# Kernel tuning notes

Measured on AMD Instinct MI355X. Metric: run time of the kernel, lower is better.

The kernel has to match this reference:

```python
import jax, jax.numpy as jnp
import numpy as np

B, L, LP, N, D, H, NL = 8, 24, 48, 325, 128, 8, 3
DFF = 4 * D          # d_ff = 4*d_model
ORDER, SUP = 2, 2    # diffusion order, support_len (1 static + 1 adaptive)
KC = ORDER * SUP + 1 # 5 concatenated diffusion channels
E = D // H


def setup_inputs() -> dict:
    key = jax.random.key(0)
    ks = iter(jax.random.split(key, 48))
    g = lambda shape: jax.random.normal(next(ks), shape, dtype=jnp.float32) * 0.02
    return {
        "x": jax.random.normal(next(ks), (B, L, N, D), dtype=jnp.float32),
        "memory": jax.random.normal(next(ks), (B, LP, N, D), dtype=jnp.float32),
        "data": jax.random.normal(next(ks), (B, L, N, D), dtype=jnp.float32),
        "support": jax.random.uniform(next(ks), (N, N), dtype=jnp.float32) / N,
        # [layer, 0=self/1=cross, ...] attention projections
        "Wq": g((NL, 2, D, D)), "bq": jnp.zeros((NL, 2, D), jnp.float32),
        "Wk": g((NL, 2, D, D)), "bk": jnp.zeros((NL, 2, D), jnp.float32),
        "Wv": g((NL, 2, D, D)), "bv": jnp.zeros((NL, 2, D), jnp.float32),
        "Wo": g((NL, 2, D, D)), "bo": jnp.zeros((NL, 2, D), jnp.float32),
        "W1": g((NL, D, DFF)), "b1": jnp.zeros((NL, DFF), jnp.float32),
        "W2": g((NL, DFF, D)), "b2": jnp.zeros((NL, D), jnp.float32),
        "W3": g((NL, D, N)),   "b3": jnp.zeros((NL, N), jnp.float32),
        "lng": jnp.ones((NL, 3, D), jnp.float32), "lnb": jnp.zeros((NL, 3, D), jnp.float32),
        # one GCN (1x1-conv mlp) per output timestep per layer
        "gcnW": g((NL, L, KC * D, D)), "gcnb": jnp.zeros((NL, L, D), jnp.float32),
        "skW": g((NL, D, D)), "skb": jnp.zeros((NL, D), jnp.float32),
        "outg": jnp.ones((D,), jnp.float32), "outb": jnp.zeros((D,), jnp.float32),
    }


def _ln(x, g, b, eps=1e-5):
    mu = x.mean(-1, keepdims=True)
    xc = x - mu
    v = (xc * xc).mean(-1, keepdims=True)
    return xc * jax.lax.rsqrt(v + eps) * g + b


def _lin_attn(qx, kx, Wq, bq, Wk, bk, Wv, bv, Wo, bo):
    # linear attention with elu+1 feature map over flattened (time*node) tokens
    Bq, S, _ = qx.shape
    T = kx.shape[1]
    q = (qx @ Wq + bq).reshape(Bq, S, H, E)
    k = (kx @ Wk + bk).reshape(Bq, T, H, E)
    v = (kx @ Wv + bv).reshape(Bq, T, H, E)
    qp = jax.nn.elu(q) + 1.0
    kp = jax.nn.elu(k) + 1.0
    kv = jnp.einsum('bthe,bthd->bhed', kp, v)
    z = 1.0 / (jnp.einsum('bshe,bhe->bsh', qp, kp.sum(1)) + 1e-6)
    out = jnp.einsum('bshe,bhed,bsh->bshd', qp, kv, z).reshape(Bq, S, D)
    return out @ Wo + bo


def _forward(x, memory, data, support, Wq, bq, Wk, bk, Wv, bv, Wo, bo,
             W1, b1, W2, b2, W3, b3, lng, lnb, gcnW, gcnb, skW, skb, outg, outb):
    skip = 0.0
    dtm = data.transpose(0, 1, 3, 2)          # [B,L,C=D,N] channels-first node features
    s1 = jnp.einsum('blcn,nm->blcm', dtm, support)
    s2 = jnp.einsum('blcn,nm->blcm', s1, support)
    for i in range(NL):
        # self-attention (tokens = L*N)
        xf = x.reshape(B, L * N, D)
        sa = _lin_attn(xf, xf, Wq[i, 0], bq[i, 0], Wk[i, 0], bk[i, 0],
                       Wv[i, 0], bv[i, 0], Wo[i, 0], bo[i, 0])
        x = _ln(x + sa.reshape(B, L, N, D), lng[i, 0], lnb[i, 0])
        # cross-attention to memory (tokens = LP*N)
        xf = x.reshape(B, L * N, D)
        mf = memory.reshape(B, LP * N, D)
        ca = _lin_attn(xf, mf, Wq[i, 1], bq[i, 1], Wk[i, 1], bk[i, 1],
                       Wv[i, 1], bv[i, 1], Wo[i, 1], bo[i, 1])
        x = _ln(x + ca.reshape(B, L, N, D), lng[i, 1], lnb[i, 1])
        # FFN + adaptive adjacency head
        y = jax.nn.gelu(jnp.einsum('blnd,df->blnf', x, W1[i]) + b1[i], approximate=False)
        y = jnp.einsum('blnf,fd->blnd', y, W2[i]) + b2[i]
        As = jnp.einsum('blnd,dm->blnm', y, W3[i]) + b3[i]   # [B,L,N,N] per-step adjacency
        # multi-support diffusion GCN, vectorized over all L timesteps
        a1 = jnp.einsum('blcn,blnm->blcm', dtm, As)
        a2 = jnp.einsum('blcn,blnm->blcm', a1, As)
        h = jnp.concatenate([dtm, s1, s2, a1, a2], axis=2)   # [B,L,KC*D,N]
        dts = jnp.einsum('blcn,lco->blno', h, gcnW[i]) + gcnb[i][None, :, None, :]
        x = _ln(x + y, lng[i, 2], lnb[i, 2])
        # 1x1 skip conv + accumulate
        skip = skip + jnp.einsum('blnd,do->blno', dts, skW[i]) + skb[i]
    return _ln(jax.nn.relu(skip), outg, outb)


def reference(x, memory, data, support, Wq, bq, Wk, bk, Wv, bv, Wo, bo,
              W1, b1, W2, b2, W3, b3, lng, lnb, gcnW, gcnb, skW, skb, outg, outb):
    return _forward(x, memory, data, support, Wq, bq, Wk, bk, Wv, bv, Wo, bo,
                    W1, b1, W2, b2, W3, b3, lng, lnb, gcnW, gcnb, skW, skb, outg, outb)
```

## Files before the change

kernel.cpp:

```cpp
#include <hip/hip_runtime.h>
#include <hip/hip_bf16.h>
#include <math.h>

#define B_   8
#define L_   24
#define LP_  48
#define N_   325
#define D_   128
#define H_   8
#define NL_  3
#define DFF_ 512

typedef __attribute__((ext_vector_type(8))) short s16x8;
typedef __attribute__((ext_vector_type(4))) float f32x4;
typedef __hip_bfloat16 bf16;

static const int  ROWS    = B_ * L_ * N_;
static const int  T_SELF  = L_ * N_;
static const int  T_CROSS = LP_ * N_;
static const long long U_ = (long long)T_SELF * D_;
static const long long SZ = (long long)B_ * U_;

enum { EPI_NONE = 0, EPI_ELU1 = 1, EPI_GELU = 2 };

struct MOut { void* d[3]; int ldc_[3]; int flg[3]; };

__device__ __forceinline__ float apply_epi(float v, int epi) {
    if (epi == EPI_ELU1) return (v > 0.f) ? (v + 1.f) : expf(v);
    if (epi == EPI_GELU) return 0.5f * v * (1.f + erff(v * 0.70710678118654752f));
    return v;
}

template<int ABF>
__global__ __launch_bounds__(256) void gk64(
    const void* __restrict__ Av, const bf16* __restrict__ Bt,
    const float* __restrict__ bias, void* __restrict__ Cv,
    int M, int Nc, int K,
    long long sA, long long sB, long long sC,
    int lda, int ldb, int ldc,
    int bmod, long long sBias, int accum, int epi, int obf, int rowbias, int npad)
{
    const int batch = blockIdx.z;
    const int m0 = blockIdx.x * 64, n0 = blockIdx.y * 64;
    const int tid = threadIdx.x, lane = tid & 63;
    const int w = tid >> 6, wm = w >> 1, wn = w & 1;
    const int r16 = lane & 15, kb = lane >> 4;

    __shared__ __align__(16) bf16 shm[64 * 144];

    const float* Af = ABF ? nullptr : ((const float*)Av + (long long)batch * sA);
    const bf16*  Ab = ABF ? ((const bf16*)Av + (long long)batch * sA) : nullptr;
    const bf16*  Bp = Bt + (long long)(batch % bmod) * sB;

    f32x4 acc[2][2];
#pragma unroll
    for (int i = 0; i < 2; ++i)
#pragma unroll
        for (int j = 0; j < 2; ++j) acc[i][j] = f32x4{0.f, 0.f, 0.f, 0.f};

    for (int k0 = 0; k0 < K; k0 += 64) {
#pragma unroll
        for (int s = 0; s < 2; ++s) {
            int slot = tid + s * 256;
            int row = slot >> 3, kg = slot & 7;
            int m = m0 + row, k = k0 + kg * 8;
            union { s16x8 v; bf16 h[8]; } val;
            if (m < M) {
                if (ABF) {
                    val.v = *(const s16x8*)(Ab + (long long)m * lda + k);
                } else {
                    f32x4 v0 = *(const f32x4*)(Af + (long long)m * lda + k);
                    f32x4 v1 = *(const f32x4*)(Af + (long long)m * lda + k + 4);
#pragma unroll
                    for (int e = 0; e < 4; ++e) {
                        val.h[e]     = __float2bfloat16(v0[e]);
                        val.h[e + 4] = __float2bfloat16(v1[e]);
                    }
                }
            } else {
#pragma unroll
                for (int e = 0; e < 8; ++e) val.h[e] = __float2bfloat16(0.f);
            }
            *(s16x8*)&shm[row * 72 + kg * 8] = val.v;
        }
#pragma unroll
        for (int s = 0; s < 2; ++s) {
            int slot = tid + s * 256;
            int row = slot >> 3, kg = slot & 7;
            int n = n0 + row, k = k0 + kg * 8;
            union { s16x8 v; bf16 h[8]; } val;
            if (n < Nc) {
                val.v = *(const s16x8*)(Bp + (long long)n * ldb + k);
            } else {
#pragma unroll
                for (int e = 0; e < 8; ++e) val.h[e] = __float2bfloat16(0.f);
            }
            *(s16x8*)&shm[4608 + row * 72 + kg * 8] = val.v;
        }
        __syncthreads();
#pragma unroll
        for (int kh = 0; kh < 2; ++kh) {
            s16x8 av[2], bv[2];
#pragma unroll
            for (int mi = 0; mi < 2; ++mi)
                av[mi] = *(const s16x8*)&shm[(wm * 32 + mi * 16 + r16) * 72 + kh * 32 + kb * 8];
#pragma unroll
            for (int ni = 0; ni < 2; ++ni)
                bv[ni] = *(const s16x8*)&shm[4608 + (wn * 32 + ni * 16 + r16) * 72 + kh * 32 + kb * 8];
#pragma unroll
            for (int mi = 0; mi < 2; ++mi)
#pragma unroll
                for (int ni = 0; ni < 2; ++ni)
                    acc[mi][ni] = __builtin_amdgcn_mfma_f32_16x16x32_bf16(
                        av[mi], bv[ni], acc[mi][ni], 0, 0, 0);
        }
        __syncthreads();
    }

    const float* bp = bias ? (bias + (long long)(batch % bmod) * sBias) : nullptr;
    if (obf) {
        bf16* Cb = (bf16*)Cv + (long long)batch * sC;
#pragma unroll
        for (int mi = 0; mi < 2; ++mi)
#pragma unroll
            for (int ni = 0; ni < 2; ++ni)
#pragma unroll
                for (int rr = 0; rr < 4; ++rr) {
                    int row = wm * 32 + mi * 16 + kb * 4 + rr;
                    int col = wn * 32 + ni * 16 + r16;
                    int m = m0 + row, n = n0 + col;
                    float v = 0.f;
                    if (m < M && n < Nc) {
                        v = acc[mi][ni][rr];
                        if (bp) v += rowbias ? bp[m] : bp[n];
                        v = apply_epi(v, epi);
                    }
                    shm[row * 72 + col] = __float2bfloat16(v);
                }
        __syncthreads();
#pragma unroll
        for (int it = 0; it < 2; ++it) {
            int row = (tid >> 3) + it * 32;
            int col = (tid & 7) * 8;
            int m = m0 + row, nglob = n0 + col;
            if (m < M && nglob < npad)
                *(s16x8*)(Cb + (long long)m * ldc + nglob) = *(const s16x8*)&shm[row * 72 + col];
        }
        return;
    }

    float* Cf = (float*)Cv + (long long)batch * sC;
#pragma unroll
    for (int mi = 0; mi < 2; ++mi) {
#pragma unroll
        for (int ni = 0; ni < 2; ++ni) {
#pragma unroll
            for (int rr = 0; rr < 4; ++rr) {
                int m = m0 + wm * 32 + mi * 16 + kb * 4 + rr;
                int n = n0 + wn * 32 + ni * 16 + r16;
                if (m >= M || n >= Nc) continue;
                float v = acc[mi][ni][rr];
                if (bp) v += rowbias ? bp[m] : bp[n];
                v = apply_epi(v, epi);
                long long ci = (long long)m * ldc + n;
                if (accum) Cf[ci] += v; else Cf[ci] = v;
            }
        }
    }
}

template<int ABF>
__global__ __launch_bounds__(256) void gk64m(
    const void* __restrict__ Av, const bf16* __restrict__ Bt,
    const float* __restrict__ bias, MOut mo, int M, int K, int lda, int ldb)
{
    const int bn = blockIdx.y;
    const int m0 = blockIdx.x * 64, n0 = bn * 64;
    const int tid = threadIdx.x, lane = tid & 63;
    const int w = tid >> 6, wm = w >> 1, wn = w & 1;
    const int r16 = lane & 15, kb = lane >> 4;

    __shared__ __align__(16) bf16 shm[64 * 144];

    const float* Af = ABF ? nullptr : (const float*)Av;
    const bf16*  Ab = ABF ? (const bf16*)Av : nullptr;

    f32x4 acc[2][2];
#pragma unroll
    for (int i = 0; i < 2; ++i)
#pragma unroll
        for (int j = 0; j < 2; ++j) acc[i][j] = f32x4{0.f, 0.f, 0.f, 0.f};

    for (int k0 = 0; k0 < K; k0 += 64) {
#pragma unroll
        for (int s = 0; s < 2; ++s) {
            int slot = tid + s * 256;
            int row = slot >> 3, kg = slot & 7;
            int m = m0 + row, k = k0 + kg * 8;
            union { s16x8 v; bf16 h[8]; } val;
            if (m < M) {
                if (ABF) {
                    val.v = *(const s16x8*)(Ab + (long long)m * lda + k);
                } else {
                    f32x4 v0 = *(const f32x4*)(Af + (long long)m * lda + k);
                    f32x4 v1 = *(const f32x4*)(Af + (long long)m * lda + k + 4);
#pragma unroll
                    for (int e = 0; e < 4; ++e) {
                        val.h[e]     = __float2bfloat16(v0[e]);
                        val.h[e + 4] = __float2bfloat16(v1[e]);
                    }
                }
            } else {
#pragma unroll
                for (int e = 0; e < 8; ++e) val.h[e] = __float2bfloat16(0.f);
            }
            *(s16x8*)&shm[row * 72 + kg * 8] = val.v;
        }
#pragma unroll
        for (int s = 0; s < 2; ++s) {
            int slot = tid + s * 256;
            int row = slot >> 3, kg = slot & 7;
            int n = n0 + row, k = k0 + kg * 8;
            *(s16x8*)&shm[4608 + row * 72 + kg * 8] =
                *(const s16x8*)(Bt + (long long)n * ldb + k);
        }
        __syncthreads();
#pragma unroll
        for (int kh = 0; kh < 2; ++kh) {
            s16x8 av[2], bv[2];
#pragma unroll
            for (int mi = 0; mi < 2; ++mi)
                av[mi] = *(const s16x8*)&shm[(wm * 32 + mi * 16 + r16) * 72 + kh * 32 + kb * 8];
#pragma unroll
            for (int ni = 0; ni < 2; ++ni)
                bv[ni] = *(const s16x8*)&shm[4608 + (wn * 32 + ni * 16 + r16) * 72 + kh * 32 + kb * 8];
#pragma unroll
            for (int mi = 0; mi < 2; ++mi)
#pragma unroll
                for (int ni = 0; ni < 2; ++ni)
                    acc[mi][ni] = __builtin_amdgcn_mfma_f32_16x16x32_bf16(
                        av[mi], bv[ni], acc[mi][ni], 0, 0, 0);
        }
        __syncthreads();
    }

    const int oi = bn >> 1;
    const int epi_ = mo.flg[oi];
    bf16* Cb = (bf16*)mo.d[oi];
    const int ldcc = mo.ldc_[oi];
    const int cbase = (bn & 1) * 64;
#pragma unroll
    for (int mi = 0; mi < 2; ++mi)
#pragma unroll
        for (int ni = 0; ni < 2; ++ni)
#pragma unroll
            for (int rr = 0; rr < 4; ++rr) {
                int row = wm * 32 + mi * 16 + kb * 4 + rr;
                int col = wn * 32 + ni * 16 + r16;
                int m = m0 + row;
                float v = 0.f;
                if (m < M) {
                    v = acc[mi][ni][rr] + bias[n0 + col];
                    v = apply_epi(v, epi_);
                }
                shm[row * 72 + col] = __float2bfloat16(v);
            }
    __syncthreads();
#pragma unroll
    for (int it = 0; it < 2; ++it) {
        int row = (tid >> 3) + it * 32;
        int col = (tid & 7) * 8;
        int m = m0 + row;
        if (m < M)
            *(s16x8*)(Cb + (long long)m * ldcc + cbase + col) = *(const s16x8*)&shm[row * 72 + col];
    }
}

static inline void gemm64(hipStream_t st, int abf, const void* A, const bf16* Bt,
                          const float* bias, void* C,
                          int M, int Nc, int K,
                          long long sA, long long sB, long long sC,
                          int lda, int ldb, int ldc,
                          int z, int bmod, long long sBias, int accum, int epi, int obf,
                          int rowbias = 0, int npad = 0)
{
    if (npad < Nc) npad = Nc;
    dim3 g((M + 63) / 64, (npad + 63) / 64, z);
    if (abf) gk64<1><<<g,256,0,st>>>(A,Bt,bias,C,M,Nc,K,sA,sB,sC,lda,ldb,ldc,bmod,sBias,accum,epi,obf,rowbias,npad);
    else     gk64<0><<<g,256,0,st>>>(A,Bt,bias,C,M,Nc,K,sA,sB,sC,lda,ldb,ldc,bmod,sBias,accum,epi,obf,rowbias,npad);
}

static inline void gemm3_64(hipStream_t st, int abf, const void* A, const bf16* Bt,
                            const float* bias, const MOut& mo, int M, int Nc, int K,
                            int lda, int ldb)
{
    dim3 g((M + 63) / 64, Nc / 64, 1);
    if (abf) gk64m<1><<<g,256,0,st>>>(A,Bt,bias,mo,M,K,lda,ldb);
    else     gk64m<0><<<g,256,0,st>>>(A,Bt,bias,mo,M,K,lda,ldb);
}

template<int SBF>
__global__ __launch_bounds__(256) void tconv(
    const void* __restrict__ srcv, bf16* __restrict__ dst,
    int R, int C, int lds_, long long sS, int rbound, int drs, long long sD)
{
    const int bz = blockIdx.z;
    const float* sf = SBF ? nullptr : ((const float*)srcv + (long long)bz * sS);
    const bf16* sb = SBF ? ((const bf16*)srcv + (long long)bz * sS) : nullptr;
    bf16* dp = dst + (long long)bz * sD;
    __shared__ float t[32][33];
    const int r0 = blockIdx.x * 32, c0 = blockIdx.y * 32;
    for (int i = threadIdx.y; i < 32; i += 8) {
        int r = r0 + i, c = c0 + threadIdx.x;
        float v = 0.f;
        if (r < R && c < C)
            v = SBF ? __bfloat162float(sb[(long long)r * lds_ + c]) : sf[(long long)r * lds_ + c];
        t[i][threadIdx.x] = v;
    }
    __syncthreads();
    for (int i = threadIdx.y; i < 32; i += 8) {
        int c = c0 + i, r = r0 + threadIdx.x;
        if (c < C && r < rbound) dp[(long long)c * drs + r] = __float2bfloat16(t[threadIdx.x][i]);
    }
}

__global__ __launch_bounds__(256) void conv_k(
    const float* __restrict__ src, bf16* __restrict__ dst,
    long long total, int C, int slds, int dldd)
{
    for (long long idx = blockIdx.x * 256LL + threadIdx.x; idx < total;
         idx += (long long)gridDim.x * 256) {
        long long r = idx / C; int c = (int)(idx - r * C);
        dst[r * dldd + c] = __float2bfloat16(src[r * slds + c]);
    }
}

__global__ __launch_bounds__(256) void gsum_k(
    const bf16* __restrict__ gskt, bf16* __restrict__ gsum, long long per)
{
    for (long long j = blockIdx.x * 256LL + threadIdx.x; j < per;
         j += (long long)gridDim.x * 256) {
        float a = __bfloat162float(gskt[j]) + __bfloat162float(gskt[per + j])
                + __bfloat162float(gskt[2 * per + j]);
        gsum[j] = __float2bfloat16(a);
    }
}

__global__ __launch_bounds__(128) void bsk_k(
    const float* __restrict__ gcnb, const float* __restrict__ skW,
    const float* __restrict__ skb, float* __restrict__ out)
{
    const int l = blockIdx.x, o = threadIdx.x;
    float acc = 0.f;
    for (int i = 0; i < NL_; ++i) {
        acc += skb[i * 128 + o];
        const float* gb = gcnb + (i * 24 + l) * 128;
        const float* sw = skW + i * 16384;
        for (int c = 0; c < 128; ++c) acc += gb[c] * sw[c * 128 + o];
    }
    out[l * 128 + o] = acc;
}

__global__ __launch_bounds__(384) void cbias_k(
    const float* __restrict__ bq, const float* __restrict__ bk,
    const float* __restrict__ bv, float* __restrict__ bqkv)
{
    const int wi = blockIdx.x, j = threadIdx.x;
    float v = (j < 128) ? bq[wi * 128 + j] : (j < 256) ? bk[wi * 128 + j - 128] : bv[wi * 128 + j - 256];
    bqkv[wi * 384 + j] = v;
}

__global__ __launch_bounds__(256) void kv_part_bf16(
    const bf16* __restrict__ kp, const bf16* __restrict__ vp,
    float* __restrict__ part, int T, int TC)
{
    const int z = blockIdx.z, h = blockIdx.y, tc = blockIdx.x;
    kp += (long long)z * T * D_;
    vp += (long long)z * T * D_;
    const int t0 = tc * 512;
    const int tend = min(T, t0 + 512);
    const int tid = threadIdx.x;
    const int e = tid >> 4, d = tid & 15;
    __shared__ float sk[64][16];
    __shared__ float sv[64][16];
    float acc = 0.f, asum = 0.f;
    for (int tb = t0; tb < tend; tb += 64) {
#pragma unroll
        for (int r = 0; r < 4; ++r) {
            int idx = tid + r * 256, tt = idx >> 4, c = idx & 15;
            int t = tb + tt;
            float kk = 0.f, vv = 0.f;
            if (t < tend) {
                long long gi = (long long)t * D_ + h * 16 + c;
                kk = __bfloat162float(kp[gi]);
                vv = __bfloat162float(vp[gi]);
            }
            sk[tt][c] = kk; sv[tt][c] = vv;
        }
        __syncthreads();
#pragma unroll 8
        for (int tt = 0; tt < 64; ++tt) {
            float ke = sk[tt][e];
            acc  = fmaf(ke, sv[tt][d], acc);
            asum += ke;
        }
        __syncthreads();
    }
    float* pp = part + (((long long)z * TC + tc) * H_ + h) * 272;
    pp[e * 16 + d] = acc;
    if (d == 0) pp[256 + e] = asum;
}

__global__ __launch_bounds__(256) void kv_reduce2(
    const float* __restrict__ part, float* __restrict__ kv,
    float* __restrict__ ksum, int b0, int TC)
{
    const int h = blockIdx.x, z = blockIdx.y, b = b0 + z;
    const float* pz = part + (long long)z * TC * H_ * 272;
    const int tid = threadIdx.x, e = tid >> 4, d = tid & 15;
    float acc = 0.f;
    for (int tc = 0; tc < TC; ++tc) acc += pz[((long long)tc * H_ + h) * 272 + e * 16 + d];
    kv[((long long)(b * H_ + h) * 16 + e) * 16 + d] = acc;
    if (d == 0) {
        float s = 0.f;
        for (int tc = 0; tc < TC; ++tc) s += pz[((long long)tc * H_ + h) * 272 + 256 + e];
        ksum[(b * H_ + h) * 16 + e] = s;
    }
}

__global__ __launch_bounds__(256) void attn_out_bf(
    const bf16* __restrict__ qp, const float* __restrict__ kv,
    const float* __restrict__ ksum, bf16* __restrict__ out)
{
    const int row = blockIdx.x * 2 + threadIdx.y;
    const int o = threadIdx.x;
    const int h = o >> 4, dp = o & 15;
    __shared__ float sq[2][D_];
    const int b = row / T_SELF;
    sq[threadIdx.y][o] = __bfloat162float(qp[(long long)row * D_ + o]);
    __syncthreads();
    const float* ks  = ksum + (b * H_ + h) * 16;
    const float* kvp = kv + (long long)(b * H_ + h) * 256 + dp;
    float den = 1e-6f, acc = 0.f;
#pragma unroll
    for (int e = 0; e < 16; ++e) {
        float q = sq[threadIdx.y][h * 16 + e];
        den = fmaf(q, ks[e], den);
        acc = fmaf(q, kvp[e * 16], acc);
    }
    out[(long long)row * D_ + o] = __float2bfloat16(acc / den);
}

template<int XBF, int OBF>
__global__ __launch_bounds__(256) void addln_k(
    const void* __restrict__ xin, const bf16* __restrict__ addend,
    const float* __restrict__ g, const float* __restrict__ beta,
    void* __restrict__ outp, int relu_mode)
{
    const int row = blockIdx.x * 4 + threadIdx.y;
    const int lane = threadIdx.x;
    const long long base = (long long)row * D_;
    float v0, v1;
    if (XBF) {
        v0 = __bfloat162float(((const bf16*)xin)[base + lane]);
        v1 = __bfloat162float(((const bf16*)xin)[base + lane + 64]);
    } else {
        v0 = ((const float*)xin)[base + lane];
        v1 = ((const float*)xin)[base + lane + 64];
    }
    if (addend) {
        v0 += __bfloat162float(addend[base + lane]);
        v1 += __bfloat162float(addend[base + lane + 64]);
    }
    if (relu_mode) { v0 = fmaxf(v0, 0.f); v1 = fmaxf(v1, 0.f); }
    float s = v0 + v1;
#pragma unroll
    for (int off = 32; off; off >>= 1) s += __shfl_xor(s, off);
    const float mean = s * (1.f / 128.f);
    const float c0 = v0 - mean, c1 = v1 - mean;
    float vs = c0 * c0 + c1 * c1;
#pragma unroll
    for (int off = 32; off; off >>= 1) vs += __shfl_xor(vs, off);
    const float rstd = rsqrtf(vs * (1.f / 128.f) + 1e-5f);
    const float r0 = c0 * rstd * g[lane] + beta[lane];
    const float r1 = c1 * rstd * g[lane + 64] + beta[lane + 64];
    if (OBF) {
        ((bf16*)outp)[base + lane]      = __float2bfloat16(r0);
        ((bf16*)outp)[base + lane + 64] = __float2bfloat16(r1);
    } else {
        ((float*)outp)[base + lane]      = r0;
        ((float*)outp)[base + lane + 64] = r1;
    }
}

extern "C" void kernel_launch(void* const* d_in, const int* in_sizes, int n_in,
                              void* d_out, int out_size, void* d_ws, size_t ws_size,
                              hipStream_t stream)
{
    (void)in_sizes; (void)n_in; (void)out_size; (void)ws_size;

    const float* x_in    = (const float*)d_in[0];
    const float* mem     = (const float*)d_in[1];
    const float* data    = (const float*)d_in[2];
    const float* support = (const float*)d_in[3];
    const float* Wq  = (const float*)d_in[4];
    const float* bq  = (const float*)d_in[5];
    const float* Wk  = (const float*)d_in[6];
    const float* bk  = (const float*)d_in[7];
    const float* Wv  = (const float*)d_in[8];
    const float* bv  = (const float*)d_in[9];
    const float* Wo  = (const float*)d_in[10];
    const float* bo  = (const float*)d_in[11];
    const float* W1  = (const float*)d_in[12];
    const float* b1  = (const float*)d_in[13];
    const float* W2  = (const float*)d_in[14];
    const float* b2  = (const float*)d_in[15];
    const float* W3  = (const float*)d_in[16];
    const float* b3  = (const float*)d_in[17];
    const float* lng = (const float*)d_in[18];
    const float* lnb = (const float*)d_in[19];
    const float* gcnW= (const float*)d_in[20];
    const float* gcnb= (const float*)d_in[21];
    const float* skW = (const float*)d_in[22];
    const float* skb = (const float*)d_in[23];
    const float* outg= (const float*)d_in[24];
    const float* outb= (const float*)d_in[25];

    float* ws = (float*)d_ws;
    bf16*  Xb16 = (bf16*)ws;
    float* POOL = ws + 4000000LL;
    bf16*  PB   = (bf16*)POOL;
    bf16*  WBF  = (bf16*)(ws + 18800000LL);
    float* BQKV = ws + 23275008LL;
    float* BSK  = ws + 23277504LL;
    float* KVB  = ws + 23280576LL;
    float* KSB  = ws + 23296960LL;

    bf16* WQKVT = WBF + 0;
    bf16* WOT   = WBF + 294912;
    bf16* W1T   = WBF + 393216;
    bf16* W2T   = WBF + 589824;
    bf16* W3T   = WBF + 786432;
    bf16* SKWT  = WBF + 911232;
    bf16* SUPT  = WBF + 960384;
    bf16* GSKT  = WBF + 1085184;
    bf16* GSUM  = WBF + 6983424;

    float* SKIP = (float*)d_out;
    const int BIG = 1 << 30;
    dim3 blk(32, 8);
    auto TG = [](int rb, int C, int z) { return dim3((rb + 31) / 32, (C + 31) / 32, z); };

    tconv<0><<<TG(128,128,6),blk,0,stream>>>(Wq, WQKVT,          128,128,128, 16384, 128,128, 49152);
    tconv<0><<<TG(128,128,6),blk,0,stream>>>(Wk, WQKVT + 16384,  128,128,128, 16384, 128,128, 49152);
    tconv<0><<<TG(128,128,6),blk,0,stream>>>(Wv, WQKVT + 32768,  128,128,128, 16384, 128,128, 49152);
    tconv<0><<<TG(128,128,6),blk,0,stream>>>(Wo, WOT,            128,128,128, 16384, 128,128, 16384);
    tconv<0><<<TG(128,512,3),blk,0,stream>>>(W1, W1T,            128,512,512, 65536, 128,128, 65536);
    tconv<0><<<TG(512,128,3),blk,0,stream>>>(W2, W2T,            512,128,128, 65536, 512,512, 65536);
    tconv<0><<<TG(128,325,3),blk,0,stream>>>(W3, W3T,            128,325,325, 41600, 128,128, 41600);
    tconv<0><<<TG(128,128,3),blk,0,stream>>>(skW, SKWT,          128,128,128, 16384, 128,128, 16384);
    tconv<0><<<TG(384,325,1),blk,0,stream>>>(support, SUPT,      325,325,325, 0,     384,384, 0);
    bf16* gcnWbf = PB;
    conv_k<<<4096,256,0,stream>>>(gcnW, gcnWbf, 5898240LL, 128, 128, 128);
    for (int i = 0; i < NL_; ++i)
        gemm64(stream, 1, SKWT + i*16384, gcnWbf + (long long)i*1966080, nullptr,
               GSKT + (long long)i*1966080,
               128, 640, 128, 0, 81920, 81920, 128, 128, 640, 24, BIG, 0, 0, EPI_NONE, 1);
    gsum_k<<<2048,256,0,stream>>>(GSKT, GSUM, 1966080LL);
    bsk_k<<<24,128,0,stream>>>(gcnb, skW, skb, BSK);
    cbias_k<<<6,384,0,stream>>>(bq, bk, bv, BQKV);
    hipMemsetAsync(SKIP, 0, (size_t)SZ * sizeof(float), stream);

    for (int c = 0; c < 2; ++c) {
        const int b0 = c * 4;
        const float* datab = data + (long long)b0 * U_;
        bf16* Hs    = PB + 0;
        bf16* DTB   = PB + 12000000LL;
        bf16* s1_cm = PB + 16800000LL;
        conv_k<<<2048,256,0,stream>>>(datab, Hs, 96LL*41600, 128, 128, 384);
        tconv<0><<<TG(384,128,96),blk,0,stream>>>(datab, DTB, 325,128,128, 41600, 384,384, 49152);
        gemm64(stream, 1, DTB, SUPT, nullptr, s1_cm, 128,325,384,
               49152, 0, 49152, 384,384,384, 96, 1, 0, 0, EPI_NONE, 1, 0, 384);
        tconv<1><<<TG(128,325,96),blk,0,stream>>>(s1_cm, Hs + 128, 128,325,384, 49152, 128,384, 124800);
        gemm64(stream, 1, SUPT, s1_cm, nullptr, Hs + 256, 325,128,384,
               0, 49152, 124800, 384,384,384, 96, BIG, 0, 0, EPI_NONE, 1);
        gemm64(stream, 1, Hs, GSUM, BSK, SKIP + (long long)b0*U_,
               325,128,384, 124800, 81920, 41600, 384, 640, 128, 96, 24, 128, 1, EPI_NONE, 0);
    }

    for (int i = 0; i < NL_; ++i) {
        {
            const int wi = i * 2;
            bf16* Q  = PB + 0;
            bf16* KB = PB + 8000000LL;
            bf16* VB = PB + 16000000LL;
            float* PART = POOL + 12000000LL;
            bf16* OB = PB + 8000000LL;
            MOut mo{};
            mo.d[0] = Q;  mo.ldc_[0] = 128; mo.flg[0] = EPI_ELU1;
            mo.d[1] = KB; mo.ldc_[1] = 128; mo.flg[1] = EPI_ELU1;
            mo.d[2] = VB; mo.ldc_[2] = 128; mo.flg[2] = EPI_NONE;
            gemm3_64(stream, (i == 0) ? 0 : 1, (i == 0) ? (const void*)x_in : (const void*)Xb16,
                     WQKVT + (long long)wi*49152, BQKV + wi*384, mo, ROWS, 384, 128, 128, 128);
            kv_part_bf16<<<dim3(16,H_,8),256,0,stream>>>(KB, VB, PART, T_SELF, 16);
            kv_reduce2<<<dim3(H_,8),256,0,stream>>>(PART, KVB, KSB, 0, 16);
            attn_out_bf<<<ROWS/2, dim3(128,2),0,stream>>>(Q, KVB, KSB, Q);
            gemm64(stream, 1, Q, WOT + (long long)wi*16384, bo + wi*128, OB,
                   ROWS, 128, 128, 0,0,0, 128,128,128, 1,1,0, 0, EPI_NONE, 1);
            if (i == 0) addln_k<0,1><<<ROWS/4, dim3(64,4),0,stream>>>(
                x_in, OB, lng + (i*3)*128, lnb + (i*3)*128, Xb16, 0);
            else        addln_k<1,1><<<ROWS/4, dim3(64,4),0,stream>>>(
                Xb16, OB, lng + (i*3)*128, lnb + (i*3)*128, Xb16, 0);
        }

        {
            const int wi = i * 2 + 1;
            for (int c = 0; c < 2; ++c) {
                const int b0 = c * 4;
                bf16* KB = PB + 0;
                bf16* VB = PB + 8000000LL;
                float* PART = POOL + 12000000LL;
                MOut mo{};
                mo.d[0] = KB; mo.ldc_[0] = 128; mo.flg[0] = EPI_ELU1;
                mo.d[1] = VB; mo.ldc_[1] = 128; mo.flg[1] = EPI_NONE;
                gemm3_64(stream, 0, mem + (long long)b0 * T_CROSS * D_,
                         WQKVT + (long long)wi*49152 + 16384, BQKV + wi*384 + 128, mo,
                         4*T_CROSS, 256, 128, 128, 128);
                kv_part_bf16<<<dim3(31,H_,4),256,0,stream>>>(KB, VB, PART, T_CROSS, 31);
                kv_reduce2<<<dim3(H_,4),256,0,stream>>>(PART, KVB, KSB, b0, 31);
            }
            bf16* Q  = PB + 0;
            bf16* OB = PB + 8000000LL;
            gemm64(stream, 1, Xb16, WQKVT + (long long)wi*49152, BQKV + wi*384, Q,
                   ROWS, 128, 128, 0,0,0, 128,128,128, 1,1,0, 0, EPI_ELU1, 1);
            attn_out_bf<<<ROWS/2, dim3(128,2),0,stream>>>(Q, KVB, KSB, Q);
            gemm64(stream, 1, Q, WOT + (long long)wi*16384, bo + wi*128, OB,
                   ROWS, 128, 128, 0,0,0, 128,128,128, 1,1,0, 0, EPI_NONE, 1);
            addln_k<1,1><<<ROWS/4, dim3(64,4),0,stream>>>(
                Xb16, OB, lng + (i*3+1)*128, lnb + (i*3+1)*128, Xb16, 0);
        }

        for (int c = 0; c < 2; ++c) {
            const int b0 = c * 4;
            bf16* Xb = Xb16 + (long long)b0 * U_;

            bf16* FFH   = PB + 0;
            bf16* Ybf   = PB + 16000000LL;
            bf16* AST   = PB + 0;
            bf16* DTB   = PB + 12000000LL;
            bf16* a1_cm = PB + 16800000LL;
            bf16* Hd    = PB + 21600000LL;

            gemm64(stream, 1, Xb, W1T + (long long)i*65536, b1 + i*512, FFH,
                   4*T_SELF, 512, 128, 0,0,0, 128,128,512, 1,1,0, 0, EPI_GELU, 1);
            gemm64(stream, 1, FFH, W2T + (long long)i*65536, b2 + i*128, Ybf,
                   4*T_SELF, 128, 512, 0,0,0, 512,512,128, 1,1,0, 0, EPI_NONE, 1);
            addln_k<1,1><<<4*T_SELF/4, dim3(64,4),0,stream>>>(
                Xb, Ybf, lng + (i*3+2)*128, lnb + (i*3+2)*128, Xb, 0);
            gemm64(stream, 1, W3T + (long long)i*41600, Ybf, b3 + i*325, AST,
                   325, 325, 128, 0, 41600, 124800, 128, 128, 384, 96, BIG, 0, 0, EPI_NONE, 1, 1, 384);
            tconv<0><<<TG(384,128,96),blk,0,stream>>>(data + (long long)b0*U_, DTB,
                  325,128,128, 41600, 384,384, 49152);
            gemm64(stream, 1, DTB, AST, nullptr, a1_cm, 128,325,384,
                   49152, 124800, 49152, 384,384,384, 96, BIG, 0, 0, EPI_NONE, 1, 0, 384);
            tconv<1><<<TG(128,325,96),blk,0,stream>>>(a1_cm, Hd, 128,325,384, 49152, 128,256, 83200);
            gemm64(stream, 1, AST, a1_cm, nullptr, Hd + 128, 325,128,384,
                   124800, 49152, 83200, 384,384,256, 96, BIG, 0, 0, EPI_NONE, 1);
            gemm64(stream, 1, Hd, GSKT + (long long)i*1966080 + 384, nullptr,
                   SKIP + (long long)b0*U_, 325,128,256,
                   83200, 81920, 41600, 256, 640, 128, 96, 24, 0, 1, EPI_NONE, 0);
        }
    }

    addln_k<0,0><<<ROWS/4, dim3(64,4),0,stream>>>(SKIP, nullptr, outg, outb, SKIP, 1);
}
```

Before: 2.257 ms.

## Load A tile once per block and sweep all output column blocks for K=128 GEMMs

Adds a GEMM kernel for K=128 that stages the full 64x128 A row-tile in shared memory once, then loops over every 64-wide column block of the weight matrix, keeping all accumulators in registers. It replaces the QKV, cross KV, Q, output-projection and FFN-up GEMMs, which previously launched one block per column tile and reloaded or re-converted A each time. This removes redundant A traffic and fp32-to-bf16 conversion, at the cost of far fewer blocks, higher register pressure (up to 8x2x2 accumulators) and a serialized epilogue per column block.

```diff
diff --git a/kernel.cpp b/kernel.cpp
--- a/kernel.cpp
+++ b/kernel.cpp
@@ -23,12 +23,142 @@
 
 enum { EPI_NONE = 0, EPI_ELU1 = 1, EPI_GELU = 2 };
 
-struct MOut { void* d[3]; int ldc_[3]; int flg[3]; };
+struct MOut8 { void* d[8]; int ldc_[8]; int cb[8]; int flg[8]; };
 
 __device__ __forceinline__ float apply_epi(float v, int epi) {
     if (epi == EPI_ELU1) return (v > 0.f) ? (v + 1.f) : expf(v);
     if (epi == EPI_GELU) return 0.5f * v * (1.f + erff(v * 0.70710678118654752f));
     return v;
+}
+
+template<int ABF, int NL>
+__global__ __launch_bounds__(256) void gkA(
+    const void* __restrict__ Av, const bf16* __restrict__ Bt,
+    const float* __restrict__ bias, MOut8 mo, int M, int lda, int ldb)
+{
+    const int m0 = blockIdx.x * 64;
+    const int tid = threadIdx.x, lane = tid & 63;
+    const int w = tid >> 6, wm = w >> 1, wn = w & 1;
+    const int r16 = lane & 15, kb = lane >> 4;
+
+    __shared__ __align__(16) bf16 shA[64 * 136];
+    __shared__ __align__(16) bf16 shB[64 * 136];
+
+    const float* Af = ABF ? nullptr : (const float*)Av;
+    const bf16*  Ab = ABF ? (const bf16*)Av : nullptr;
+
+#pragma unroll
+    for (int s = 0; s < 4; ++s) {
+        int slot = tid + s * 256;
+        int row = slot >> 4, kg = slot & 15;
+        int m = m0 + row, k = kg * 8;
+        union { s16x8 v; bf16 h[8]; } val;
+        if (m < M) {
+            if (ABF) {
+                val.v = *(const s16x8*)(Ab + (long long)m * lda + k);
+            } else {
+                f32x4 v0 = *(const f32x4*)(Af + (long long)m * lda + k);
+                f32x4 v1 = *(const f32x4*)(Af + (long long)m * lda + k + 4);
+#pragma unroll
+                for (int e = 0; e < 4; ++e) {
+                    val.h[e]     = __float2bfloat16(v0[e]);
+                    val.h[e + 4] = __float2bfloat16(v1[e]);
+                }
+            }
+        } else {
+#pragma unroll
+            for (int e = 0; e < 8; ++e) val.h[e] = __float2bfloat16(0.f);
+        }
+        *(s16x8*)&shA[row * 136 + kg * 8] = val.v;
+    }
+
+    f32x4 acc[NL][2][2];
+#pragma unroll
+    for (int nb = 0; nb < NL; ++nb)
+#pragma unroll
+        for (int i = 0; i < 2; ++i)
+#pragma unroll
+            for (int j = 0; j < 2; ++j) acc[nb][i][j] = f32x4{0.f, 0.f, 0.f, 0.f};
+
+#pragma unroll
+    for (int nb = 0; nb < NL; ++nb) {
+#pragma unroll
+        for (int s = 0; s < 4; ++s) {
+            int slot = tid + s * 256;
+            int row = slot >> 4, kg = slot & 15;
+            int n = nb * 64 + row, k = kg * 8;
+            *(s16x8*)&shB[row * 136 + kg * 8] = *(const s16x8*)(Bt + (long long)n * ldb + k);
+        }
+        __syncthreads();
+#pragma unroll
+        for (int ks = 0; ks < 4; ++ks) {
+            s16x8 av[2], bv[2];
+#pragma unroll
+            for (int mi = 0; mi < 2; ++mi)
+                av[mi] = *(const s16x8*)&shA[(wm * 32 + mi * 16 + r16) * 136 + ks * 32 + kb * 8];
+#pragma unroll
+            for (int ni = 0; ni < 2; ++ni)
+                bv[ni] = *(const s16x8*)&shB[(wn * 32 + ni * 16 + r16) * 136 + ks * 32 + kb * 8];
+#pragma unroll
+            for (int mi = 0; mi < 2; ++mi)
+#pragma unroll
+                for (int ni = 0; ni < 2; ++ni)
+                    acc[nb][mi][ni] = __builtin_amdgcn_mfma_f32_16x16x32_bf16(
+                        av[mi], bv[ni], acc[nb][mi][ni], 0, 0, 0);
+        }
+        __syncthreads();
+    }
+
+#pragma unroll
+    for (int nb = 0; nb < NL; ++nb) {
+        const int epi_ = mo.flg[nb];
+        bf16* Cb = (bf16*)mo.d[nb];
+        const int ldcc = mo.ldc_[nb];
+        const int cbase = mo.cb[nb];
+#pragma unroll
+        for (int mi = 0; mi < 2; ++mi)
+#pragma unroll
+            for (int ni = 0; ni < 2; ++ni)
+#pragma unroll
+                for (int rr = 0; rr < 4; ++rr) {
+                    int row = wm * 32 + mi * 16 + kb * 4 + rr;
+                    int col = wn * 32 + ni * 16 + r16;
+                    int m = m0 + row;
+                    float v = 0.f;
+                    if (m < M) {
+                        v = acc[nb][mi][ni][rr] + bias[nb * 64 + col];
+                        v = apply_epi(v, epi_);
+                    }
+                    shB[row * 72 + col] = __float2bfloat16(v);
+                }
+        __syncthreads();
+#pragma unroll
+        for (int it = 0; it < 2; ++it) {
+            int row = (tid >> 3) + it * 32;
+            int col = (tid & 7) * 8;
+            int m = m0 + row;
+            if (m < M)
+                *(s16x8*)(Cb + (long long)m * ldcc + cbase + col) = *(const s16x8*)&shB[row * 72 + col];
+        }
+        __syncthreads();
+    }
+}
+
+static inline void gemmA(hipStream_t st, int abf, int nl, const void* A, const bf16* Bt,
+                         const float* bias, const MOut8& mo, int M, int lda, int ldb)
+{
+    dim3 g((M + 63) / 64);
+    if (abf) {
+        if (nl == 2)      gkA<1,2><<<g,256,0,st>>>(A,Bt,bias,mo,M,lda,ldb);
+        else if (nl == 4) gkA<1,4><<<g,256,0,st>>>(A,Bt,bias,mo,M,lda,ldb);
+        else if (nl == 6) gkA<1,6><<<g,256,0,st>>>(A,Bt,bias,mo,M,lda,ldb);
+        else              gkA<1,8><<<g,256,0,st>>>(A,Bt,bias,mo,M,lda,ldb);
+    } else {
+        if (nl == 2)      gkA<0,2><<<g,256,0,st>>>(A,Bt,bias,mo,M,lda,ldb);
+        else if (nl == 4) gkA<0,4><<<g,256,0,st>>>(A,Bt,bias,mo,M,lda,ldb);
+        else if (nl == 6) gkA<0,6><<<g,256,0,st>>>(A,Bt,bias,mo,M,lda,ldb);
+        else              gkA<0,8><<<g,256,0,st>>>(A,Bt,bias,mo,M,lda,ldb);
+    }
 }
 
 template<int ABF>
@@ -169,113 +299,6 @@
     }
 }
 
-template<int ABF>
-__global__ __launch_bounds__(256) void gk64m(
-    const void* __restrict__ Av, const bf16* __restrict__ Bt,
-    const float* __restrict__ bias, MOut mo, int M, int K, int lda, int ldb)
-{
-    const int bn = blockIdx.y;
-    const int m0 = blockIdx.x * 64, n0 = bn * 64;
-    const int tid = threadIdx.x, lane = tid & 63;
-    const int w = tid >> 6, wm = w >> 1, wn = w & 1;
-    const int r16 = lane & 15, kb = lane >> 4;
-
-    __shared__ __align__(16) bf16 shm[64 * 144];
-
-    const float* Af = ABF ? nullptr : (const float*)Av;
-    const bf16*  Ab = ABF ? (const bf16*)Av : nullptr;
-
-    f32x4 acc[2][2];
-#pragma unroll
-    for (int i = 0; i < 2; ++i)
-#pragma unroll
-        for (int j = 0; j < 2; ++j) acc[i][j] = f32x4{0.f, 0.f, 0.f, 0.f};
-
-    for (int k0 = 0; k0 < K; k0 += 64) {
-#pragma unroll
-        for (int s = 0; s < 2; ++s) {
-            int slot = tid + s * 256;
-            int row = slot >> 3, kg = slot & 7;
-            int m = m0 + row, k = k0 + kg * 8;
-            union { s16x8 v; bf16 h[8]; } val;
-            if (m < M) {
-                if (ABF) {
-                    val.v = *(const s16x8*)(Ab + (long long)m * lda + k);
-                } else {
-                    f32x4 v0 = *(const f32x4*)(Af + (long long)m * lda + k);
-                    f32x4 v1 = *(const f32x4*)(Af + (long long)m * lda + k + 4);
-#pragma unroll
-                    for (int e = 0; e < 4; ++e) {
-                        val.h[e]     = __float2bfloat16(v0[e]);
-                        val.h[e + 4] = __float2bfloat16(v1[e]);
-                    }
-                }
-            } else {
-#pragma unroll
-                for (int e = 0; e < 8; ++e) val.h[e] = __float2bfloat16(0.f);
-            }
-            *(s16x8*)&shm[row * 72 + kg * 8] = val.v;
-        }
-#pragma unroll
-        for (int s = 0; s < 2; ++s) {
-            int slot = tid + s * 256;
-            int row = slot >> 3, kg = slot & 7;
-            int n = n0 + row, k = k0 + kg * 8;
-            *(s16x8*)&shm[4608 + row * 72 + kg * 8] =
-                *(const s16x8*)(Bt + (long long)n * ldb + k);
-        }
-        __syncthreads();
-#pragma unroll
-        for (int kh = 0; kh < 2; ++kh) {
-            s16x8 av[2], bv[2];
-#pragma unroll
-            for (int mi = 0; mi < 2; ++mi)
-                av[mi] = *(const s16x8*)&shm[(wm * 32 + mi * 16 + r16) * 72 + kh * 32 + kb * 8];
-#pragma unroll
-            for (int ni = 0; ni < 2; ++ni)
-                bv[ni] = *(const s16x8*)&shm[4608 + (wn * 32 + ni * 16 + r16) * 72 + kh * 32 + kb * 8];
-#pragma unroll
-            for (int mi = 0; mi < 2; ++mi)
-#pragma unroll
-                for (int ni = 0; ni < 2; ++ni)
-                    acc[mi][ni] = __builtin_amdgcn_mfma_f32_16x16x32_bf16(
-                        av[mi], bv[ni], acc[mi][ni], 0, 0, 0);
-        }
-        __syncthreads();
-    }
-
-    const int oi = bn >> 1;
-    const int epi_ = mo.flg[oi];
-    bf16* Cb = (bf16*)mo.d[oi];
-    const int ldcc = mo.ldc_[oi];
-    const int cbase = (bn & 1) * 64;
-#pragma unroll
-    for (int mi = 0; mi < 2; ++mi)
-#pragma unroll
-        for (int ni = 0; ni < 2; ++ni)
-#pragma unroll
-            for (int rr = 0; rr < 4; ++rr) {
-                int row = wm * 32 + mi * 16 + kb * 4 + rr;
-                int col = wn * 32 + ni * 16 + r16;
-                int m = m0 + row;
-                float v = 0.f;
-                if (m < M) {
-                    v = acc[mi][ni][rr] + bias[n0 + col];
-                    v = apply_epi(v, epi_);
-                }
-                shm[row * 72 + col] = __float2bfloat16(v);
-            }
-    __syncthreads();
-#pragma unroll
-    for (int it = 0; it < 2; ++it) {
-        int row = (tid >> 3) + it * 32;
-        int col = (tid & 7) * 8;
-        int m = m0 + row;
-        if (m < M)
-            *(s16x8*)(Cb + (long long)m * ldcc + cbase + col) = *(const s16x8*)&shm[row * 72 + col];
-    }
-}
-
 static inline void gemm64(hipStream_t st, int abf, const void* A, const bf16* Bt,
                           const float* bias, void* C,
                           int M, int Nc, int K,
@@ -288,15 +311,6 @@
     dim3 g((M + 63) / 64, (npad + 63) / 64, z);
     if (abf) gk64<1><<<g,256,0,st>>>(A,Bt,bias,C,M,Nc,K,sA,sB,sC,lda,ldb,ldc,bmod,sBias,accum,epi,obf,rowbias,npad);
     else     gk64<0><<<g,256,0,st>>>(A,Bt,bias,C,M,Nc,K,sA,sB,sC,lda,ldb,ldc,bmod,sBias,accum,epi,obf,rowbias,npad);
-}
-
-static inline void gemm3_64(hipStream_t st, int abf, const void* A, const bf16* Bt,
-                            const float* bias, const MOut& mo, int M, int Nc, int K,
-                            int lda, int ldb)
-{
-    dim3 g((M + 63) / 64, Nc / 64, 1);
-    if (abf) gk64m<1><<<g,256,0,st>>>(A,Bt,bias,mo,M,K,lda,ldb);
-    else     gk64m<0><<<g,256,0,st>>>(A,Bt,bias,mo,M,K,lda,ldb);
 }
 
 template<int SBF>
@@ -596,17 +610,25 @@
             bf16* VB = PB + 16000000LL;
             float* PART = POOL + 12000000LL;
             bf16* OB = PB + 8000000LL;
-            MOut mo{};
-            mo.d[0] = Q;  mo.ldc_[0] = 128; mo.flg[0] = EPI_ELU1;
-            mo.d[1] = KB; mo.ldc_[1] = 128; mo.flg[1] = EPI_ELU1;
-            mo.d[2] = VB; mo.ldc_[2] = 128; mo.flg[2] = EPI_NONE;
-            gemm3_64(stream, (i == 0) ? 0 : 1, (i == 0) ? (const void*)x_in : (const void*)Xb16,
-                     WQKVT + (long long)wi*49152, BQKV + wi*384, mo, ROWS, 384, 128, 128, 128);
+            MOut8 mo{};
+            mo.d[0] = Q;  mo.cb[0] = 0;  mo.flg[0] = EPI_ELU1;
+            mo.d[1] = Q;  mo.cb[1] = 64; mo.flg[1] = EPI_ELU1;
+            mo.d[2] = KB; mo.cb[2] = 0;  mo.flg[2] = EPI_ELU1;
+            mo.d[3] = KB; mo.cb[3] = 64; mo.flg[3] = EPI_ELU1;
+            mo.d[4] = VB; mo.cb[4] = 0;  mo.flg[4] = EPI_NONE;
+            mo.d[5] = VB; mo.cb[5] = 64; mo.flg[5] = EPI_NONE;
+            for (int t = 0; t < 6; ++t) mo.ldc_[t] = 128;
+            gemmA(stream, (i == 0) ? 0 : 1, 6,
+                  (i == 0) ? (const void*)x_in : (const void*)Xb16,
+                  WQKVT + (long long)wi*49152, BQKV + wi*384, mo, ROWS, 128, 128);
             kv_part_bf16<<<dim3(16,H_,8),256,0,stream>>>(KB, VB, PART, T_SELF, 16);
             kv_reduce2<<<dim3(H_,8),256,0,stream>>>(PART, KVB, KSB, 0, 16);
             attn_out_bf<<<ROWS/2, dim3(128,2),0,stream>>>(Q, KVB, KSB, Q);
-            gemm64(stream, 1, Q, WOT + (long long)wi*16384, bo + wi*128, OB,
-                   ROWS, 128, 128, 0,0,0, 128,128,128, 1,1,0, 0, EPI_NONE, 1);
+            MOut8 mw{};
+            mw.d[0] = OB; mw.cb[0] = 0;  mw.flg[0] = EPI_NONE;
+            mw.d[1] = OB; mw.cb[1] = 64; mw.flg[1] = EPI_NONE;
+            mw.ldc_[0] = mw.ldc_[1] = 128;
+            gemmA(stream, 1, 2, Q, WOT + (long long)wi*16384, bo + wi*128, mw, ROWS, 128, 128);
             if (i == 0) addln_k<0,1><<<ROWS/4, dim3(64,4),0,stream>>>(
                 x_in, OB, lng + (i*3)*128, lnb + (i*3)*128, Xb16, 0);
             else        addln_k<1,1><<<ROWS/4, dim3(64,4),0,stream>>>(
@@ -620,22 +642,31 @@
                 bf16* KB = PB + 0;
                 bf16* VB = PB + 8000000LL;
                 float* PART = POOL + 12000000LL;
-                MOut mo{};
-                mo.d[0] = KB; mo.ldc_[0] = 128; mo.flg[0] = EPI_ELU1;
-                mo.d[1] = VB; mo.ldc_[1] = 128; mo.flg[1] = EPI_NONE;
-                gemm3_64(stream, 0, mem + (long long)b0 * T_CROSS * D_,
-                         WQKVT + (long long)wi*49152 + 16384, BQKV + wi*384 + 128, mo,
-                         4*T_CROSS, 256, 128, 128, 128);
+                MOut8 mo{};
+                mo.d[0] = KB; mo.cb[0] = 0;  mo.flg[0] = EPI_ELU1;
+                mo.d[1] = KB; mo.cb[1] = 64; mo.flg[1] = EPI_ELU1;
+                mo.d[2] = VB; mo.cb[2] = 0;  mo.flg[2] = EPI_NONE;
+                mo.d[3] = VB; mo.cb[3] = 64; mo.flg[3] = EPI_NONE;
+                for (int t = 0; t < 4; ++t) mo.ldc_[t] = 128;
+                gemmA(stream, 0, 4, mem + (long long)b0 * T_CROSS * D_,
+                      WQKVT + (long long)wi*49152 + 16384, BQKV + wi*384 + 128, mo,
+                      4*T_CROSS, 128, 128);
                 kv_part_bf16<<<dim3(31,H_,4),256,0,stream>>>(KB, VB, PART, T_CROSS, 31);
                 kv_reduce2<<<dim3(H_,4),256,0,stream>>>(PART, KVB, KSB, b0, 31);
             }
             bf16* Q  = PB + 0;
             bf16* OB = PB + 8000000LL;
-            gemm64(stream, 1, Xb16, WQKVT + (long long)wi*49152, BQKV + wi*384, Q,
-                   ROWS, 128, 128, 0,0,0, 128,128,128, 1,1,0, 0, EPI_ELU1, 1);
+            MOut8 mq{};
+            mq.d[0] = Q; mq.cb[0] = 0;  mq.flg[0] = EPI_ELU1;
+            mq.d[1] = Q; mq.cb[1] = 64; mq.flg[1] = EPI_ELU1;
+            mq.ldc_[0] = mq.ldc_[1] = 128;
+            gemmA(stream, 1, 2, Xb16, WQKVT + (long long)wi*49152, BQKV + wi*384, mq, ROWS, 128, 128);
             attn_out_bf<<<ROWS/2, dim3(128,2),0,stream>>>(Q, KVB, KSB, Q);
-            gemm64(stream, 1, Q, WOT + (long long)wi*16384, bo + wi*128, OB,
-                   ROWS, 128, 128, 0,0,0, 128,128,128, 1,1,0, 0, EPI_NONE, 1);
+            MOut8 mw{};
+            mw.d[0] = OB; mw.cb[0] = 0;  mw.flg[0] = EPI_NONE;
+            mw.d[1] = OB; mw.cb[1] = 64; mw.flg[1] = EPI_NONE;
+            mw.ldc_[0] = mw.ldc_[1] = 128;
+            gemmA(stream, 1, 2, Q, WOT + (long long)wi*16384, bo + wi*128, mw, ROWS, 128, 128);
             addln_k<1,1><<<ROWS/4, dim3(64,4),0,stream>>>(
                 Xb16, OB, lng + (i*3+1)*128, lnb + (i*3+1)*128, Xb16, 0);
         }
@@ -651,8 +682,9 @@
             bf16* a1_cm = PB + 16800000LL;
             bf16* Hd    = PB + 21600000LL;
 
-            gemm64(stream, 1, Xb, W1T + (long long)i*65536, b1 + i*512, FFH,
-                   4*T_SELF, 512, 128, 0,0,0, 128,128,512, 1,1,0, 0, EPI_GELU, 1);
+            MOut8 m1{};
+            for (int t = 0; t < 8; ++t) { m1.d[t] = FFH; m1.cb[t] = t * 64; m1.ldc_[t] = 512; m1.flg[t] = EPI_GELU; }
+            gemmA(stream, 1, 8, Xb, W1T + (long long)i*65536, b1 + i*512, m1, 4*T_SELF, 128, 128);
             gemm64(stream, 1, FFH, W2T + (long long)i*65536, b2 + i*128, Ybf,
                    4*T_SELF, 128, 512, 0,0,0, 512,512,128, 1,1,0, 0, EPI_NONE, 1);
             addln_k<1,1><<<4*T_SELF/4, dim3(64,4),0,stream>>>(
```

After: 3.388 ms. +50.1%, slower.
